# Performance work log

Hardware: AMD Instinct MI355X
Metric: run time of the kernel (lower is better)

Reference implementation:

```python
import jax, jax.numpy as jnp
import numpy as np

DIM = 1024        # model dim
HEADS = 1         # num_heads (fc1 in_features==1 forces this)
HDIM = DIM // HEADS
INNER = 16        # dim_inner
B, L = 2, 4096
ROPE_BASE = 32.0


def _apply_rope(x, pos, base):
    # x: [b, l, h, d]; standard rotate-half RoPE
    d = x.shape[-1]
    inv_freq = base ** (-jnp.arange(0, d, 2, dtype=jnp.float32) / d)   # [d/2]
    ang = pos[:, None].astype(jnp.float32) * inv_freq                  # [l, d/2]
    emb = jnp.concatenate([ang, ang], axis=-1)                         # [l, d]
    cos = jnp.cos(emb)[None, :, None, :].astype(x.dtype)
    sin = jnp.sin(emb)[None, :, None, :].astype(x.dtype)
    x1, x2 = x[..., : d // 2], x[..., d // 2:]
    rot = jnp.concatenate([-x2, x1], axis=-1)
    return x * cos + rot * sin


def setup_inputs() -> dict:
    key = jax.random.key(0)
    ks = jax.random.split(key, 7)
    hidden_states = jax.random.normal(ks[0], (B, L, DIM), dtype=jnp.float32)
    Wq = jax.random.normal(ks[1], (DIM, DIM), dtype=jnp.float32) * 0.02
    Wk = jax.random.normal(ks[2], (DIM, DIM), dtype=jnp.float32) * 0.02
    fc1_w = jax.random.normal(ks[3], (INNER, 1), dtype=jnp.float32) * 0.1
    fc1_b = jax.random.normal(ks[4], (INNER,), dtype=jnp.float32) * 0.1
    fc2_w = jax.random.normal(ks[5], (DIM, INNER), dtype=jnp.float32) * 0.1
    fc2_b = jax.random.normal(ks[6], (DIM,), dtype=jnp.float32) * 0.1
    return {"hidden_states": hidden_states, "Wq": Wq, "Wk": Wk,
            "fc1_w": fc1_w, "fc1_b": fc1_b, "fc2_w": fc2_w, "fc2_b": fc2_b}


def reference(hidden_states, Wq, Wk, fc1_w, fc1_b, fc2_w, fc2_b):
    b, l, _ = hidden_states.shape
    # projections, cast to bf16 as in the torch module
    q = (hidden_states @ Wq.T).reshape(b, l, HEADS, HDIM).astype(jnp.bfloat16)
    k = (hidden_states @ Wk.T).reshape(b, l, HEADS, HDIM).astype(jnp.bfloat16)
    pos = jnp.arange(l)
    q = _apply_rope(q, pos, ROPE_BASE)
    k = _apply_rope(k, pos, ROPE_BASE)
    # causal exp(QK) with NO softmax normalization; accumulate in fp32
    scores = jnp.einsum('bqhd,bkhd->bhqk',
                        q.astype(jnp.float32), k.astype(jnp.float32)) / (HDIM ** 0.5)
    causal = jnp.tril(jnp.ones((l, l), dtype=bool))                    # [l, l]
    exp_qk = jnp.where(causal[None, None], jnp.exp(scores), 0.0)       # [b, h, l, l]
    o = jnp.swapaxes(exp_qk.sum(axis=-1), 1, 2)                        # [b, l, h]
    # small MLP: h(=1) -> INNER -> DIM
    o = jax.nn.relu(o @ fc1_w.T + fc1_b)
    return o @ fc2_w.T + fc2_b                                         # [b, l, DIM]
```

## Files before the change

kernel.cpp:

```cpp
#include <hip/hip_runtime.h>
#include <hip/hip_bf16.h>

typedef __bf16 bf16_t;
typedef __bf16 bf16x4 __attribute__((ext_vector_type(4)));
typedef __bf16 bf16x8 __attribute__((ext_vector_type(8)));
typedef float f32x4 __attribute__((ext_vector_type(4)));

#define B_   2
#define L_   4096
#define DIM_ 1024
#define M_   (B_ * L_)
#define MT_  (L_ / 128)
#define NTASK_ ((MT_ * (MT_ + 1)) / 2)

__device__ __forceinline__ void ld_g2l_16(const bf16_t* g, bf16_t* l) {
  __builtin_amdgcn_global_load_lds(
      (__attribute__((address_space(1))) void*)g,
      (__attribute__((address_space(3))) void*)l, 16, 0, 0);
}

__global__ void cvt_f32_bf16(const float* __restrict__ src,
                             bf16_t* __restrict__ dst, int n4) {
  int i = blockIdx.x * blockDim.x + threadIdx.x;
  if (i < n4) {
    float4 v = ((const float4*)src)[i];
    bf16x4 o = { (bf16_t)v.x, (bf16_t)v.y, (bf16_t)v.z, (bf16_t)v.w };
    ((bf16x4*)dst)[i] = o;
  }
}

__device__ __forceinline__ void mfma_bt_core(const bf16_t* __restrict__ A,
                                             const bf16_t* __restrict__ B,
                                             int K, bf16_t* As, bf16_t* Bs,
                                             f32x4 (&acc)[4][4]) {
  const int tid  = threadIdx.x;
  const int wave = tid >> 6, lane = tid & 63;
  const int quad = lane >> 4, l16 = lane & 15;
  const int wm = (wave >> 1) * 64, wn = (wave & 1) * 64;
  const int srow = lane >> 2;
  const int scol = (lane & 3) * 8;

  for (int kk = 0; kk < K; kk += 32) {
    __syncthreads();
#pragma unroll
    for (int c = 0; c < 2; ++c) {
      int seg = c * 4 + wave;
      int row = seg * 16 + srow;
      ld_g2l_16(A + (size_t)row * K + kk + scol, As + seg * 512);
      ld_g2l_16(B + (size_t)row * K + kk + scol, Bs + seg * 512);
    }
    __syncthreads();

    bf16x8 af[4], bfr[4];
#pragma unroll
    for (int i = 0; i < 4; ++i) {
      af[i]  = *(const bf16x8*)(As + (wm + i * 16 + l16) * 32 + quad * 8);
      bfr[i] = *(const bf16x8*)(Bs + (wn + i * 16 + l16) * 32 + quad * 8);
    }
#pragma unroll
    for (int i = 0; i < 4; ++i)
#pragma unroll
      for (int j = 0; j < 4; ++j)
        acc[i][j] = __builtin_amdgcn_mfma_f32_16x16x32_bf16(af[i], bfr[j],
                                                            acc[i][j], 0, 0, 0);
  }
}

__global__ __launch_bounds__(256)
void proj_gemm(const bf16_t* __restrict__ A, const bf16_t* __restrict__ Wqb,
               const bf16_t* __restrict__ Wkb, bf16_t* __restrict__ Cq,
               bf16_t* __restrict__ Ck) {
  const int K = DIM_, N = DIM_;
  const bf16_t* Bm = (blockIdx.z == 0) ? Wqb : Wkb;
  bf16_t* Cm = (blockIdx.z == 0) ? Cq : Ck;
  __shared__ __attribute__((aligned(16))) bf16_t As[128 * 32];
  __shared__ __attribute__((aligned(16))) bf16_t Bs[128 * 32];
  const int tid = threadIdx.x;
  const int wave = tid >> 6, lane = tid & 63;
  const int quad = lane >> 4, l16 = lane & 15;
  const int wm = (wave >> 1) * 64, wn = (wave & 1) * 64;
  const int m0 = blockIdx.y * 128, n0 = blockIdx.x * 128;

  f32x4 acc[4][4] = {};
  mfma_bt_core(A + (size_t)m0 * K, Bm + (size_t)n0 * K, K, As, Bs, acc);

#pragma unroll
  for (int i = 0; i < 4; ++i)
#pragma unroll
    for (int j = 0; j < 4; ++j)
#pragma unroll
      for (int r = 0; r < 4; ++r) {
        int m = m0 + wm + i * 16 + quad * 4 + r;
        int n = n0 + wn + j * 16 + l16;
        Cm[(size_t)m * N + n] = (bf16_t)acc[i][j][r];
      }
}

__global__ void rope_kernel(bf16_t* __restrict__ x) {
  int row = blockIdx.x * 2 + (threadIdx.x >> 7);
  int j0  = (threadIdx.x & 127) * 4;
  int pos = row & (L_ - 1);
  bf16_t* p = x + (size_t)row * DIM_;
  bf16x4 v1 = *(const bf16x4*)(p + j0);
  bf16x4 v2 = *(const bf16x4*)(p + j0 + 512);
  bf16x4 o1, o2;
#pragma unroll
  for (int u = 0; u < 4; ++u) {
    int j = j0 + u;
    float ang = (float)pos * exp2f((float)j * (-5.0f / 512.0f));
    float c = cosf(ang), s = sinf(ang);
    float cb = (float)(bf16_t)c, sb = (float)(bf16_t)s;
    float x1 = (float)v1[u], x2 = (float)v2[u];
    o1[u] = (bf16_t)(x1 * cb - x2 * sb);
    o2[u] = (bf16_t)(x2 * cb + x1 * sb);
  }
  *(bf16x4*)(p + j0) = o1;
  *(bf16x4*)(p + j0 + 512) = o2;
}

__global__ void zero_f32(float* p, int n) {
  int i = blockIdx.x * blockDim.x + threadIdx.x;
  if (i < n) p[i] = 0.0f;
}

__global__ __launch_bounds__(256)
void attn_rowsum(const bf16_t* __restrict__ Q, const bf16_t* __restrict__ Kc,
                 float* __restrict__ o) {
  int t = blockIdx.x;
  int b = t / NTASK_;
  t -= b * NTASK_;
  int mt = (int)((sqrtf(8.0f * (float)t + 1.0f) - 1.0f) * 0.5f);
  while ((mt + 1) * (mt + 2) / 2 <= t) ++mt;
  while (mt * (mt + 1) / 2 > t) --mt;
  int nt = t - mt * (mt + 1) / 2;

  __shared__ __attribute__((aligned(16))) bf16_t As[128 * 32];
  __shared__ __attribute__((aligned(16))) bf16_t Bs[128 * 32];
  const int tid = threadIdx.x;
  const int wave = tid >> 6, lane = tid & 63;
  const int quad = lane >> 4, l16 = lane & 15;
  const int wm = (wave >> 1) * 64, wn = (wave & 1) * 64;

  const bf16_t* A  = Q  + (size_t)b * L_ * DIM_ + (size_t)mt * 128 * DIM_;
  const bf16_t* Bp = Kc + (size_t)b * L_ * DIM_ + (size_t)nt * 128 * DIM_;

  f32x4 acc[4][4] = {};
  mfma_bt_core(A, Bp, DIM_, As, Bs, acc);

  const bool diag = (mt == nt);
#pragma unroll
  for (int i = 0; i < 4; ++i) {
#pragma unroll
    for (int r = 0; r < 4; ++r) {
      int mrow = wm + i * 16 + quad * 4 + r;
      float sum = 0.0f;
#pragma unroll
      for (int j = 0; j < 4; ++j) {
        int ncol = wn + j * 16 + l16;
        float e = __expf(acc[i][j][r] * 0.03125f);
        if (!diag || ncol <= mrow) sum += e;
      }
      sum += __shfl_xor(sum, 1);
      sum += __shfl_xor(sum, 2);
      sum += __shfl_xor(sum, 4);
      sum += __shfl_xor(sum, 8);
      if (l16 == 0)
        atomicAdd(&o[b * L_ + mt * 128 + mrow], sum);
    }
  }
}

__global__ __launch_bounds__(256)
void mlp_out_kernel(const float* __restrict__ o, const float* __restrict__ fc1_w,
                    const float* __restrict__ fc1_b, const float* __restrict__ fc2_w,
                    const float* __restrict__ fc2_b, float* __restrict__ out) {
  const int R = 16;
  int row0 = blockIdx.x * R;
  int tid = threadIdx.x;
  __shared__ float h[R][16];
  {
    int rl = tid >> 4, i = tid & 15;
    float s = o[row0 + rl];
    h[rl][i] = fmaxf(fc1_w[i] * s + fc1_b[i], 0.0f);
  }
  __syncthreads();
  int d = tid * 4;
  float w[4][16];
#pragma unroll
  for (int c = 0; c < 4; ++c)
#pragma unroll
    for (int i = 0; i < 16; ++i) w[c][i] = fc2_w[(d + c) * 16 + i];
  float4 bb = *(const float4*)(fc2_b + d);
  for (int rl = 0; rl < R; ++rl) {
    float4 v = bb;
#pragma unroll
    for (int i = 0; i < 16; ++i) {
      float hv = h[rl][i];
      v.x += w[0][i] * hv; v.y += w[1][i] * hv;
      v.z += w[2][i] * hv; v.w += w[3][i] * hv;
    }
    *(float4*)(out + (size_t)(row0 + rl) * DIM_ + d) = v;
  }
}

extern "C" void kernel_launch(void* const* d_in, const int* in_sizes, int n_in,
                              void* d_out, int out_size, void* d_ws, size_t ws_size,
                              hipStream_t stream) {
  const float* hs    = (const float*)d_in[0];
  const float* Wq    = (const float*)d_in[1];
  const float* Wk    = (const float*)d_in[2];
  const float* fc1_w = (const float*)d_in[3];
  const float* fc1_b = (const float*)d_in[4];
  const float* fc2_w = (const float*)d_in[5];
  const float* fc2_b = (const float*)d_in[6];
  float* out = (float*)d_out;

  char* ws = (char*)d_ws;
  bf16_t* hs_bf = (bf16_t*)ws; ws += (size_t)M_ * DIM_ * 2;
  bf16_t* wq_bf = (bf16_t*)ws; ws += (size_t)DIM_ * DIM_ * 2;
  bf16_t* wk_bf = (bf16_t*)ws; ws += (size_t)DIM_ * DIM_ * 2;
  bf16_t* q_bf  = (bf16_t*)ws; ws += (size_t)M_ * DIM_ * 2;
  bf16_t* k_bf  = (bf16_t*)ws; ws += (size_t)M_ * DIM_ * 2;
  float*  o     = (float*)ws;

  cvt_f32_bf16<<<M_ * DIM_ / 4 / 256, 256, 0, stream>>>(hs, hs_bf, M_ * DIM_ / 4);
  cvt_f32_bf16<<<DIM_ * DIM_ / 4 / 256, 256, 0, stream>>>(Wq, wq_bf, DIM_ * DIM_ / 4);
  cvt_f32_bf16<<<DIM_ * DIM_ / 4 / 256, 256, 0, stream>>>(Wk, wk_bf, DIM_ * DIM_ / 4);

  dim3 gg(DIM_ / 128, M_ / 128, 2);
  proj_gemm<<<gg, 256, 0, stream>>>(hs_bf, wq_bf, wk_bf, q_bf, k_bf);

  rope_kernel<<<M_ / 2, 256, 0, stream>>>(q_bf);
  rope_kernel<<<M_ / 2, 256, 0, stream>>>(k_bf);

  zero_f32<<<M_ / 256, 256, 0, stream>>>(o, M_);
  attn_rowsum<<<B_ * NTASK_, 256, 0, stream>>>(q_bf, k_bf, o);

  mlp_out_kernel<<<M_ / 16, 256, 0, stream>>>(o, fc1_w, fc1_b, fc2_w, fc2_b, out);
}
```

Before: 255.5 us.

## Fuse RoPE into projection epilogue, interleave weight rows, double-buffer K loop

Merges the three f32-to-bf16 conversions into one launch and permutes Wq/Wk rows so rotate-half pairs land in adjacent columns. RoPE is then applied in the projection GEMM epilogue through a lane shuffle, which removes the two separate rope passes over Q and K. The GEMM core now reads the A operand straight from global memory into registers with prefetch, stages only B in double-buffered, XOR-swizzled LDS, and sets a minimum of 3 blocks per CU in the launch bounds. The zeroing kernel is replaced by hipMemsetAsync. The risks are extra sin/cos work in the epilogue and uncoalesced direct global loads of A.

```diff
diff --git a/kernel.cpp b/kernel.cpp
--- a/kernel.cpp
+++ b/kernel.cpp
@@ -19,62 +19,83 @@
       (__attribute__((address_space(3))) void*)l, 16, 0, 0);
 }
 
-__global__ void cvt_f32_bf16(const float* __restrict__ src,
-                             bf16_t* __restrict__ dst, int n4) {
+__global__ void cvt_all(const float* __restrict__ hs, const float* __restrict__ wq,
+                        const float* __restrict__ wk, bf16_t* __restrict__ hs_b,
+                        bf16_t* __restrict__ wq_b, bf16_t* __restrict__ wk_b) {
+  const int N_HS = M_ * DIM_ / 4, N_W = DIM_ * DIM_ / 4;
   int i = blockIdx.x * blockDim.x + threadIdx.x;
-  if (i < n4) {
-    float4 v = ((const float4*)src)[i];
-    bf16x4 o = { (bf16_t)v.x, (bf16_t)v.y, (bf16_t)v.z, (bf16_t)v.w };
-    ((bf16x4*)dst)[i] = o;
-  }
-}
-
-__device__ __forceinline__ void mfma_bt_core(const bf16_t* __restrict__ A,
-                                             const bf16_t* __restrict__ B,
-                                             int K, bf16_t* As, bf16_t* Bs,
-                                             f32x4 (&acc)[4][4]) {
-  const int tid  = threadIdx.x;
-  const int wave = tid >> 6, lane = tid & 63;
+  const float* s; bf16_t* d; int idx, dst;
+  if (i < N_HS) { s = hs; d = hs_b; idx = i; dst = i; }
+  else {
+    int iw = i - N_HS;
+    if (iw < N_W) { s = wq; d = wq_b; } else { s = wk; d = wk_b; iw -= N_W; }
+    idx = iw;
+    int r = iw >> 8, c4 = iw & 255;
+    int pr = (r < 512) ? 2 * r : 2 * (r - 512) + 1;
+    dst = pr * 256 + c4;
+  }
+  float4 v = ((const float4*)s)[idx];
+  bf16x4 o = { (bf16_t)v.x, (bf16_t)v.y, (bf16_t)v.z, (bf16_t)v.w };
+  ((bf16x4*)d)[dst] = o;
+}
+
+__device__ __forceinline__ void k_loop(const bf16_t* __restrict__ A,
+                                       const bf16_t* __restrict__ B,
+                                       bf16_t* Bs, f32x4 (&acc)[4][4]) {
+  const int tid = threadIdx.x, wave = tid >> 6, lane = tid & 63;
   const int quad = lane >> 4, l16 = lane & 15;
-  const int wm = (wave >> 1) * 64, wn = (wave & 1) * 64;
   const int srow = lane >> 2;
-  const int scol = (lane & 3) * 8;
-
-  for (int kk = 0; kk < K; kk += 32) {
-    __syncthreads();
+  const int scol = ((lane & 3) ^ ((lane >> 3) & 3)) * 8;
+  const int rsw  = ((l16 >> 1) & 3) * 8;
+  const int wm = (wave >> 1) * 64, wnseg = (wave & 1) * 4;
+
+  auto stage = [&](int buf, int kk) {
 #pragma unroll
     for (int c = 0; c < 2; ++c) {
       int seg = c * 4 + wave;
       int row = seg * 16 + srow;
-      ld_g2l_16(A + (size_t)row * K + kk + scol, As + seg * 512);
-      ld_g2l_16(B + (size_t)row * K + kk + scol, Bs + seg * 512);
+      ld_g2l_16(B + (size_t)row * DIM_ + kk + scol, Bs + buf * 4096 + seg * 512);
     }
+  };
+  auto loadA = [&](bf16x8 (&af)[4], int kk) {
+#pragma unroll
+    for (int i = 0; i < 4; ++i)
+      af[i] = *(const bf16x8*)(A + (size_t)(wm + i * 16 + l16) * DIM_ + kk + quad * 8);
+  };
+
+  bf16x8 af[4], afn[4];
+  stage(0, 0);
+  loadA(af, 0);
+#pragma unroll 2
+  for (int kk = 0; kk < DIM_; kk += 32) {
+    int buf = (kk >> 5) & 1;
+    int kkn = (kk + 32 < DIM_) ? kk + 32 : 0;
     __syncthreads();
-
-    bf16x8 af[4], bfr[4];
-#pragma unroll
-    for (int i = 0; i < 4; ++i) {
-      af[i]  = *(const bf16x8*)(As + (wm + i * 16 + l16) * 32 + quad * 8);
-      bfr[i] = *(const bf16x8*)(Bs + (wn + i * 16 + l16) * 32 + quad * 8);
-    }
+    stage(buf ^ 1, kkn);
+    loadA(afn, kkn);
+    bf16x8 bfr[4];
+#pragma unroll
+    for (int j = 0; j < 4; ++j)
+      bfr[j] = *(const bf16x8*)(Bs + buf * 4096 + (wnseg + j) * 512 + l16 * 32 +
+                                ((quad * 8) ^ rsw));
 #pragma unroll
     for (int i = 0; i < 4; ++i)
 #pragma unroll
       for (int j = 0; j < 4; ++j)
         acc[i][j] = __builtin_amdgcn_mfma_f32_16x16x32_bf16(af[i], bfr[j],
                                                             acc[i][j], 0, 0, 0);
-  }
-}
-
-__global__ __launch_bounds__(256)
+#pragma unroll
+    for (int i = 0; i < 4; ++i) af[i] = afn[i];
+  }
+}
+
+__global__ __launch_bounds__(256, 3)
 void proj_gemm(const bf16_t* __restrict__ A, const bf16_t* __restrict__ Wqb,
                const bf16_t* __restrict__ Wkb, bf16_t* __restrict__ Cq,
                bf16_t* __restrict__ Ck) {
-  const int K = DIM_, N = DIM_;
   const bf16_t* Bm = (blockIdx.z == 0) ? Wqb : Wkb;
   bf16_t* Cm = (blockIdx.z == 0) ? Cq : Ck;
-  __shared__ __attribute__((aligned(16))) bf16_t As[128 * 32];
-  __shared__ __attribute__((aligned(16))) bf16_t Bs[128 * 32];
+  __shared__ __attribute__((aligned(16))) bf16_t Bs[2 * 4096];
   const int tid = threadIdx.x;
   const int wave = tid >> 6, lane = tid & 63;
   const int quad = lane >> 4, l16 = lane & 15;
@@ -82,7 +103,7 @@
   const int m0 = blockIdx.y * 128, n0 = blockIdx.x * 128;
 
   f32x4 acc[4][4] = {};
-  mfma_bt_core(A + (size_t)m0 * K, Bm + (size_t)n0 * K, K, As, Bs, acc);
+  k_loop(A + (size_t)m0 * DIM_, Bm + (size_t)n0 * DIM_, Bs, acc);
 
 #pragma unroll
   for (int i = 0; i < 4; ++i)
@@ -91,81 +112,60 @@
 #pragma unroll
       for (int r = 0; r < 4; ++r) {
         int m = m0 + wm + i * 16 + quad * 4 + r;
-        int n = n0 + wn + j * 16 + l16;
-        Cm[(size_t)m * N + n] = (bf16_t)acc[i][j][r];
+        int c = n0 + wn + j * 16 + l16;
+        float val = (float)(bf16_t)acc[i][j][r];
+        float par = __shfl_xor(val, 1);
+        int t = c >> 1;
+        int pos = m & (L_ - 1);
+        float ang = (float)pos * exp2f((float)t * (-5.0f / 512.0f));
+        float cb = (float)(bf16_t)cosf(ang), sb = (float)(bf16_t)sinf(ang);
+        float ov = (c & 1) ? (val * cb + par * sb) : (val * cb - par * sb);
+        Cm[(size_t)m * DIM_ + c] = (bf16_t)ov;
       }
 }
 
-__global__ void rope_kernel(bf16_t* __restrict__ x) {
-  int row = blockIdx.x * 2 + (threadIdx.x >> 7);
-  int j0  = (threadIdx.x & 127) * 4;
-  int pos = row & (L_ - 1);
-  bf16_t* p = x + (size_t)row * DIM_;
-  bf16x4 v1 = *(const bf16x4*)(p + j0);
-  bf16x4 v2 = *(const bf16x4*)(p + j0 + 512);
-  bf16x4 o1, o2;
-#pragma unroll
-  for (int u = 0; u < 4; ++u) {
-    int j = j0 + u;
-    float ang = (float)pos * exp2f((float)j * (-5.0f / 512.0f));
-    float c = cosf(ang), s = sinf(ang);
-    float cb = (float)(bf16_t)c, sb = (float)(bf16_t)s;
-    float x1 = (float)v1[u], x2 = (float)v2[u];
-    o1[u] = (bf16_t)(x1 * cb - x2 * sb);
-    o2[u] = (bf16_t)(x2 * cb + x1 * sb);
-  }
-  *(bf16x4*)(p + j0) = o1;
-  *(bf16x4*)(p + j0 + 512) = o2;
-}
-
-__global__ void zero_f32(float* p, int n) {
-  int i = blockIdx.x * blockDim.x + threadIdx.x;
-  if (i < n) p[i] = 0.0f;
-}
-
-__global__ __launch_bounds__(256)
+__global__ __launch_bounds__(256, 3)
 void attn_rowsum(const bf16_t* __restrict__ Q, const bf16_t* __restrict__ Kc,
                  float* __restrict__ o) {
   int t = blockIdx.x;
   int b = t / NTASK_;
   t -= b * NTASK_;
-  int mt = (int)((sqrtf(8.0f * (float)t + 1.0f) - 1.0f) * 0.5f);
-  while ((mt + 1) * (mt + 2) / 2 <= t) ++mt;
-  while (mt * (mt + 1) / 2 > t) --mt;
-  int nt = t - mt * (mt + 1) / 2;
-
-  __shared__ __attribute__((aligned(16))) bf16_t As[128 * 32];
-  __shared__ __attribute__((aligned(16))) bf16_t Bs[128 * 32];
+  int mi = (int)((sqrtf(8.0f * (float)t + 1.0f) - 1.0f) * 0.5f);
+  while ((mi + 1) * (mi + 2) / 2 <= t) ++mi;
+  while (mi * (mi + 1) / 2 > t) --mi;
+  int nt = t - mi * (mi + 1) / 2;
+
+  __shared__ __attribute__((aligned(16))) bf16_t Bs[2 * 4096];
   const int tid = threadIdx.x;
   const int wave = tid >> 6, lane = tid & 63;
   const int quad = lane >> 4, l16 = lane & 15;
   const int wm = (wave >> 1) * 64, wn = (wave & 1) * 64;
 
-  const bf16_t* A  = Q  + (size_t)b * L_ * DIM_ + (size_t)mt * 128 * DIM_;
+  const bf16_t* A  = Q  + (size_t)b * L_ * DIM_ + (size_t)mi * 128 * DIM_;
   const bf16_t* Bp = Kc + (size_t)b * L_ * DIM_ + (size_t)nt * 128 * DIM_;
 
   f32x4 acc[4][4] = {};
-  mfma_bt_core(A, Bp, DIM_, As, Bs, acc);
-
-  const bool diag = (mt == nt);
+  k_loop(A, Bp, Bs, acc);
+
+  const bool masked = (nt == mi);
 #pragma unroll
   for (int i = 0; i < 4; ++i) {
 #pragma unroll
     for (int r = 0; r < 4; ++r) {
-      int mrow = wm + i * 16 + quad * 4 + r;
+      int grow = mi * 128 + wm + i * 16 + quad * 4 + r;
       float sum = 0.0f;
 #pragma unroll
       for (int j = 0; j < 4; ++j) {
-        int ncol = wn + j * 16 + l16;
+        int gcol = nt * 128 + wn + j * 16 + l16;
         float e = __expf(acc[i][j][r] * 0.03125f);
-        if (!diag || ncol <= mrow) sum += e;
+        if (!masked || gcol <= grow) sum += e;
       }
       sum += __shfl_xor(sum, 1);
       sum += __shfl_xor(sum, 2);
       sum += __shfl_xor(sum, 4);
       sum += __shfl_xor(sum, 8);
       if (l16 == 0)
-        atomicAdd(&o[b * L_ + mt * 128 + mrow], sum);
+        atomicAdd(&o[b * L_ + grow], sum);
     }
   }
 }
@@ -223,17 +223,14 @@
   bf16_t* k_bf  = (bf16_t*)ws; ws += (size_t)M_ * DIM_ * 2;
   float*  o     = (float*)ws;
 
-  cvt_f32_bf16<<<M_ * DIM_ / 4 / 256, 256, 0, stream>>>(hs, hs_bf, M_ * DIM_ / 4);
-  cvt_f32_bf16<<<DIM_ * DIM_ / 4 / 256, 256, 0, stream>>>(Wq, wq_bf, DIM_ * DIM_ / 4);
-  cvt_f32_bf16<<<DIM_ * DIM_ / 4 / 256, 256, 0, stream>>>(Wk, wk_bf, DIM_ * DIM_ / 4);
+  const int n4 = (M_ * DIM_ + 2 * DIM_ * DIM_) / 4;
+  cvt_all<<<n4 / 256, 256, 0, stream>>>(hs, Wq, Wk, hs_bf, wq_bf, wk_bf);
+
+  hipMemsetAsync(o, 0, M_ * sizeof(float), stream);
 
   dim3 gg(DIM_ / 128, M_ / 128, 2);
   proj_gemm<<<gg, 256, 0, stream>>>(hs_bf, wq_bf, wk_bf, q_bf, k_bf);
 
-  rope_kernel<<<M_ / 2, 256, 0, stream>>>(q_bf);
-  rope_kernel<<<M_ / 2, 256, 0, stream>>>(k_bf);
-
-  zero_f32<<<M_ / 256, 256, 0, stream>>>(o, M_);
   attn_rowsum<<<B_ * NTASK_, 256, 0, stream>>>(q_bf, k_bf, o);
 
   mlp_out_kernel<<<M_ / 16, 256, 0, stream>>>(o, fc1_w, fc1_b, fc2_w, fc2_b, out);
```

Measured after the change: 905.1 us. 254% more time.
